# Kernel optimization log

Measured on AMD Instinct MI355X. Metric: run time of the kernel, lower is better.

## Reference

```python
import jax, jax.numpy as jnp
import numpy as np
from jax import lax

EPS = 1e-5
T, N, E = 10, 10000, 320000
C_IN, C_HID, C_OUT = 16, 32, 16


def _stgcn_layer(x, edge_index, edge_weight, tw, tb, gw, gb, gamma, beta):
    # x: [T, N, Cin] -> temporal conv over T per node
    xc = jnp.transpose(x, (1, 2, 0))  # [N, Cin, T]
    y = lax.conv_general_dilated(xc, tw, window_strides=(1,), padding=((1, 1),),
                                 dimension_numbers=("NCH", "OIH", "NCH"))
    y = y + tb[None, :, None]
    y = jnp.clip(y, -10.0, 10.0)
    # InstanceNorm1d (affine, biased var over time axis)
    mu = jnp.mean(y, axis=-1, keepdims=True)
    var = jnp.mean((y - mu) ** 2, axis=-1, keepdims=True)
    y = (y - mu) * lax.rsqrt(var + EPS) * gamma[None, :, None] + beta[None, :, None]
    y = jax.nn.relu(y)
    h = jnp.transpose(y, (0, 2, 1))  # [N, T, C]

    n = h.shape[0]
    # GCNConv normalization (identical at every timestep -> computed once)
    ewn = jax.nn.softmax(edge_weight)  # softmax over all E edges
    loop = jnp.arange(n, dtype=edge_index.dtype)
    row = jnp.concatenate([edge_index[0], loop])  # sources (+self loops)
    col = jnp.concatenate([edge_index[1], loop])  # destinations
    w = jnp.concatenate([ewn, jnp.ones((n,), dtype=ewn.dtype)])
    deg = jax.ops.segment_sum(w, col, num_segments=n)
    dinv = jnp.where(deg > 0, lax.rsqrt(jnp.maximum(deg, EPS * 0 + 1e-30)), 0.0)
    norm = dinv[row] * w * dinv[col]  # [E+N]

    hw = jnp.einsum("ntc,cd->ntd", h, gw)  # [N, T, C]
    msg = hw[row] * norm[:, None, None]     # [E+N, T, C] gather
    agg = jax.ops.segment_sum(msg, col, num_segments=n) + gb  # scatter-add
    out = jnp.clip(jax.nn.relu(agg), -10.0, 10.0)
    return jnp.transpose(out, (1, 0, 2))  # [T, N, C]


def setup_inputs() -> dict:
    key = jax.random.key(0)
    ks = jax.random.split(key, 16)
    inp = {
        "x": jax.random.normal(ks[0], (T, N, C_IN), dtype=jnp.float32),
        "edge_index": jax.random.randint(ks[1], (2, E), 0, N, dtype=jnp.int32),
        "edge_weight": jax.random.uniform(ks[2], (E,), dtype=jnp.float32),
        # layer 1 (in -> hid)
        "l1_tw": jax.random.normal(ks[3], (C_HID, C_IN, 3), dtype=jnp.float32) * 0.02,
        "l1_tb": jnp.zeros((C_HID,), dtype=jnp.float32),
        "l1_gw": jax.random.normal(ks[4], (C_HID, C_HID), dtype=jnp.float32) * 0.1,
        "l1_gb": jnp.zeros((C_HID,), dtype=jnp.float32),
        "l1_gamma": jnp.ones((C_HID,), dtype=jnp.float32),
        "l1_beta": jnp.zeros((C_HID,), dtype=jnp.float32),
        # layer 2 (hid -> hid)
        "l2_tw": jax.random.normal(ks[5], (C_HID, C_HID, 3), dtype=jnp.float32) * 0.02,
        "l2_tb": jnp.zeros((C_HID,), dtype=jnp.float32),
        "l2_gw": jax.random.normal(ks[6], (C_HID, C_HID), dtype=jnp.float32) * 0.1,
        "l2_gb": jnp.zeros((C_HID,), dtype=jnp.float32),
        "l2_gamma": jnp.ones((C_HID,), dtype=jnp.float32),
        "l2_beta": jnp.zeros((C_HID,), dtype=jnp.float32),
        # output linear
        "out_w": jax.random.normal(ks[7], (C_HID, C_OUT), dtype=jnp.float32) * 0.1,
        "out_b": jnp.zeros((C_OUT,), dtype=jnp.float32),
    }
    return inp


def reference(x, edge_index, edge_weight,
              l1_tw, l1_tb, l1_gw, l1_gb, l1_gamma, l1_beta,
              l2_tw, l2_tb, l2_gw, l2_gb, l2_gamma, l2_beta,
              out_w, out_b):
    h = _stgcn_layer(x, edge_index, edge_weight, l1_tw, l1_tb, l1_gw, l1_gb, l1_gamma, l1_beta)
    h = _stgcn_layer(h, edge_index, edge_weight, l2_tw, l2_tb, l2_gw, l2_gb, l2_gamma, l2_beta)
    # per-timestep linear then mean over time == mean then linear, done faithfully
    outs = jnp.einsum("tnc,cd->tnd", h, out_w) + out_b
    return jnp.mean(outs, axis=0)  # [N, C_OUT]
```

## Files before the change

### kernel.cpp

```cpp
#include <hip/hip_runtime.h>
#include <hip/hip_bf16.h>
#include <string.h>


typedef __hip_bfloat16 bf16;

#define TSTEPS 10
#define TPAD 12
#define CHID 32
#define ROWELE (TSTEPS * CHID)
#define ROWW4 40

#define DEG_SHIFT 45
#define DEG_SCALE 16777216.0f
#define DEG_MASK ((1ULL << DEG_SHIFT) - 1)

__device__ __forceinline__ float b2f(bf16 v) { return __bfloat162float(v); }
__device__ __forceinline__ float ldf(const void* p, long i, int bf) {
    return bf ? __bfloat162float(((const bf16*)p)[i]) : ((const float*)p)[i];
}
__device__ __forceinline__ int detect_bf(const unsigned* gbits) {
    return (gbits[0] != 0x3F800000u) ? 1 : 0;
}
__device__ __forceinline__ float bflo(unsigned u) { return __uint_as_float(u << 16); }
__device__ __forceinline__ float bfhi(unsigned u) { return __uint_as_float(u & 0xFFFF0000u); }
__device__ __forceinline__ unsigned pack2bf(float a, float b) {
    bf16 x = __float2bfloat16(a), y = __float2bfloat16(b);
    unsigned short ux, uy;
    memcpy(&ux, &x, 2); memcpy(&uy, &y, 2);
    return (unsigned)ux | ((unsigned)uy << 16);
}
__device__ __forceinline__ unsigned short bfbits(float a) {
    bf16 x = __float2bfloat16(a);
    unsigned short u; memcpy(&u, &x, 2);
    return u;
}
__device__ __forceinline__ void accum8(float* f, uint4 u, float w) {
    f[0] += w * bflo(u.x); f[1] += w * bfhi(u.x);
    f[2] += w * bflo(u.y); f[3] += w * bfhi(u.y);
    f[4] += w * bflo(u.z); f[5] += w * bfhi(u.z);
    f[6] += w * bflo(u.w); f[7] += w * bfhi(u.w);
}
__device__ __forceinline__ unsigned long long packdeg(float e) {
    return (1ULL << DEG_SHIFT) + (unsigned long long)(e * DEG_SCALE);
}


__global__ __launch_bounds__(256) void edge_kernel(
    const void* __restrict__ ew, const unsigned* __restrict__ gbits,
    const int* __restrict__ ei,
    float* __restrict__ ewn, unsigned long long* __restrict__ packed,
    int* __restrict__ rank, float* __restrict__ sumexp, int E) {
    __shared__ float s_red[4];
    int bf = detect_bf(gbits);
    int tid = threadIdx.x;
    int i0 = (blockIdx.x * 256 + tid) * 4;
    float e0 = 0.0f, e1 = 0.0f, e2 = 0.0f, e3 = 0.0f;
    if ((E & 3) == 0 && i0 + 3 < E) {
        float w0, w1, w2, w3;
        if (bf) {
            uint2 u = ((const uint2*)ew)[i0 >> 2];
            w0 = bflo(u.x); w1 = bfhi(u.x); w2 = bflo(u.y); w3 = bfhi(u.y);
        } else {
            float4 f = ((const float4*)ew)[i0 >> 2];
            w0 = f.x; w1 = f.y; w2 = f.z; w3 = f.w;
        }
        e0 = __expf(w0); e1 = __expf(w1); e2 = __expf(w2); e3 = __expf(w3);
        int4 c4 = *(const int4*)&ei[E + i0];
        unsigned long long o0 = atomicAdd(&packed[c4.x], packdeg(e0));
        unsigned long long o1 = atomicAdd(&packed[c4.y], packdeg(e1));
        unsigned long long o2 = atomicAdd(&packed[c4.z], packdeg(e2));
        unsigned long long o3 = atomicAdd(&packed[c4.w], packdeg(e3));
        *(float4*)&ewn[i0] = make_float4(e0, e1, e2, e3);
        *(int4*)&rank[i0] = make_int4((int)(o0 >> DEG_SHIFT),
                                      (int)(o1 >> DEG_SHIFT),
                                      (int)(o2 >> DEG_SHIFT),
                                      (int)(o3 >> DEG_SHIFT));
    } else {
        float es[4] = {0, 0, 0, 0};
        for (int j = 0; j < 4; j++) {
            int i = i0 + j;
            if (i < E) {
                float e = __expf(ldf(ew, i, bf));
                es[j] = e;
                ewn[i] = e;
                unsigned long long o =
                    atomicAdd(&packed[ei[E + i]], packdeg(e));
                rank[i] = (int)(o >> DEG_SHIFT);
            }
        }
        e0 = es[0]; e1 = es[1]; e2 = es[2]; e3 = es[3];
    }
    float v = (e0 + e1) + (e2 + e3);
    for (int o = 32; o > 0; o >>= 1) v += __shfl_down(v, o);
    int lane = tid & 63, wv = tid >> 6;
    if (lane == 0) s_red[wv] = v;
    __syncthreads();
    if (tid == 0) atomicAdd(sumexp, s_red[0] + s_red[1] + s_red[2] + s_red[3]);
}


__global__ __launch_bounds__(1024) void scan_kernel(
    const unsigned long long* __restrict__ packed,
    const float* __restrict__ sumexp,
    float* __restrict__ dinv, int* __restrict__ off, int N) {
    __shared__ int s[1024];
    int tid = threadIdx.x;
    float invS = 1.0f / (*sumexp);
    for (int i = tid; i < N; i += 1024) {
        float deg = (float)(packed[i] & DEG_MASK) * (1.0f / DEG_SCALE);
        dinv[i] = rsqrtf(1.0f + deg * invS);
    }
    int chunk = (N + 1023) / 1024;
    int b0 = tid * chunk;
    int p = 0;
    for (int k = 0; k < chunk; k++) {
        int i = b0 + k;
        if (i < N) p += (int)(packed[i] >> DEG_SHIFT);
    }
    s[tid] = p;
    __syncthreads();
    for (int d = 1; d < 1024; d <<= 1) {
        int v = (tid >= d) ? s[tid - d] : 0;
        __syncthreads();
        s[tid] += v;
        __syncthreads();
    }
    int base = s[tid] - p;
    for (int k = 0; k < chunk; k++) {
        int i = b0 + k;
        if (i < N) {
            off[i] = base;
            base += (int)(packed[i] >> DEG_SHIFT);
            if (i == N - 1) off[N] = base;
        }
    }
}


template <int CIN, int LAYOUT>
__device__ __forceinline__ void conv_body(
    int bb, const void* __restrict__ in_, int bfw,
    const void* __restrict__ tw, const void* __restrict__ tb,
    const void* __restrict__ gamma, const void* __restrict__ beta,
    const void* __restrict__ gw,
    bf16* __restrict__ hw, int N, int tid) {
    constexpr int CO = CHID;
    __shared__ __align__(16) float s_in[8 * CIN * TPAD];
    __shared__ __align__(16) float s_h[8 * CO * TPAD];
    __shared__ __align__(16) unsigned s_tw01[CIN * CO];
    __shared__ __align__(16) unsigned short s_tw2[CIN * CO];
    __shared__ __align__(16) unsigned s_gwp[(CO / 2) * CO];

    int nl = tid >> 5, o = tid & 31;

    float tbv = ldf(tb, o, bfw);
    float gav = ldf(gamma, o, bfw);
    float bev = ldf(beta, o, bfw);

    for (int i = tid; i < CIN * CO; i += 256) {
        int ci = i / CO, oo = i % CO;
        long base = ((long)oo * CIN + ci) * 3;
        float w0 = ldf(tw, base, bfw);
        float w1 = ldf(tw, base + 1, bfw);
        float w2 = ldf(tw, base + 2, bfw);
        s_tw01[ci * CO + oo] = pack2bf(w0, w1);
        s_tw2[ci * CO + oo] = bfbits(w2);
    }
    for (int i = tid; i < (CO / 2) * CO; i += 256) {
        int cp = i / CO, oo = i % CO;
        s_gwp[i] = pack2bf(ldf(gw, (long)(2 * cp) * CO + oo, bfw),
                           ldf(gw, (long)(2 * cp + 1) * CO + oo, bfw));
    }

    int nb = bb * 8;

    if (LAYOUT == 0) {
        constexpr int CP = CIN / 2;
        for (int i2 = tid; i2 < 8 * TSTEPS * CP; i2 += 256) {
            int cp = i2 % CP;
            int t = (i2 / CP) % TSTEPS;
            int nn = i2 / (CP * TSTEPS);
            int n = nb + nn;
            float v0 = 0.0f, v1 = 0.0f;
            if (n < N) {
                long idx = (long)t * ((long)N * CIN) + (long)n * CIN + 2 * cp;
                if (bfw) {
                    unsigned u = ((const unsigned*)in_)[idx >> 1];
                    v0 = bflo(u); v1 = bfhi(u);
                } else {
                    float2 f = ((const float2*)in_)[idx >> 1];
                    v0 = f.x; v1 = f.y;
                }
            }
            int b = nn * (CIN * TPAD) + (2 * cp) * TPAD + t;
            s_in[b] = v0;
            s_in[b + TPAD] = v1;
        }
    } else {
        for (int i2 = tid; i2 < 8 * CIN * 5; i2 += 256) {
            int tp = i2 % 5;
            int ci = (i2 / 5) % CIN;
            int nn = i2 / (5 * CIN);
            int n = nb + nn;
            float v0 = 0.0f, v1 = 0.0f;
            if (n < N) {
                long idx = (long)n * (CIN * TSTEPS) + ci * TSTEPS + 2 * tp;
                unsigned u = ((const unsigned*)in_)[idx >> 1];
                v0 = bflo(u); v1 = bfhi(u);
            }
            int b = nn * (CIN * TPAD) + ci * TPAD + 2 * tp;
            s_in[b] = v0;
            s_in[b + 1] = v1;
        }
    }
    __syncthreads();

    int n = nb + nl;
    const float* xrow = &s_in[nl * CIN * TPAD];

    float acc[TSTEPS];
#pragma unroll
    for (int t = 0; t < TSTEPS; t++) acc[t] = tbv;

    for (int ci = 0; ci < CIN; ci++) {
        const float4* xp = (const float4*)&xrow[ci * TPAD];
        float4 A = xp[0], B = xp[1], C = xp[2];
        float xr[TSTEPS] = {A.x, A.y, A.z, A.w, B.x, B.y, B.z, B.w, C.x, C.y};
        unsigned w01 = s_tw01[ci * CO + o];
        float w0 = bflo(w01), w1 = bfhi(w01);
        float w2 = __uint_as_float(((unsigned)s_tw2[ci * CO + o]) << 16);
        acc[0] += xr[0] * w1 + xr[1] * w2;
#pragma unroll
        for (int t = 1; t < TSTEPS - 1; t++)
            acc[t] += xr[t - 1] * w0 + xr[t] * w1 + xr[t + 1] * w2;
        acc[TSTEPS - 1] += xr[TSTEPS - 2] * w0 + xr[TSTEPS - 1] * w1;
    }

#pragma unroll
    for (int t = 0; t < TSTEPS; t++) acc[t] = fminf(fmaxf(acc[t], -10.0f), 10.0f);
    float mu = 0.0f;
#pragma unroll
    for (int t = 0; t < TSTEPS; t++) mu += acc[t];
    mu *= 0.1f;
    float var = 0.0f;
#pragma unroll
    for (int t = 0; t < TSTEPS; t++) { float d = acc[t] - mu; var += d * d; }
    var *= 0.1f;
    float sc = gav * rsqrtf(var + 1e-5f);
    float h[TSTEPS];
#pragma unroll
    for (int t = 0; t < TSTEPS; t++) h[t] = fmaxf((acc[t] - mu) * sc + bev, 0.0f);

    float4* hp = (float4*)&s_h[nl * CO * TPAD + o * TPAD];
    hp[0] = make_float4(h[0], h[1], h[2], h[3]);
    hp[1] = make_float4(h[4], h[5], h[6], h[7]);
    hp[2] = make_float4(h[8], h[9], 0.0f, 0.0f);
    __syncthreads();

    float acc2[TSTEPS];
#pragma unroll
    for (int t = 0; t < TSTEPS; t++) acc2[t] = 0.0f;
    const float* hrow = &s_h[nl * CO * TPAD];
    for (int cp = 0; cp < CO / 2; cp++) {
        unsigned g2 = s_gwp[cp * CO + o];
        float g0 = bflo(g2), g1 = bfhi(g2);
        const float4* r0 = (const float4*)&hrow[(2 * cp) * TPAD];
        const float4* r1 = (const float4*)&hrow[(2 * cp + 1) * TPAD];
        float4 A0 = r0[0], B0 = r0[1], C0 = r0[2];
        float4 A1 = r1[0], B1 = r1[1], C1 = r1[2];
        acc2[0] += A0.x * g0 + A1.x * g1;
        acc2[1] += A0.y * g0 + A1.y * g1;
        acc2[2] += A0.z * g0 + A1.z * g1;
        acc2[3] += A0.w * g0 + A1.w * g1;
        acc2[4] += B0.x * g0 + B1.x * g1;
        acc2[5] += B0.y * g0 + B1.y * g1;
        acc2[6] += B0.z * g0 + B1.z * g1;
        acc2[7] += B0.w * g0 + B1.w * g1;
        acc2[8] += C0.x * g0 + C1.x * g1;
        acc2[9] += C0.y * g0 + C1.y * g1;
    }
    if (n < N) {
        unsigned* hwp = (unsigned*)hw;
        long base = (long)n * (ROWELE / 2) + o * (TSTEPS / 2);
#pragma unroll
        for (int j = 0; j < 5; j++)
            hwp[base + j] = pack2bf(acc2[2 * j], acc2[2 * j + 1]);
    }
}


__device__ __forceinline__ void fill_body(
    int bb, const int* __restrict__ ei, const float* __restrict__ ewn,
    const int* __restrict__ rank,
    const float* __restrict__ dinv, const float* __restrict__ sumexp,
    const int* __restrict__ off, int2* __restrict__ csr, int E, int tid) {
    int i0 = (bb * 256 + tid) * 4;
    if (i0 >= E) return;
    float invS = 1.0f / (*sumexp);
    if ((E & 3) == 0 && i0 + 3 < E) {
        int4 r4 = *(const int4*)&ei[i0];
        int4 c4 = *(const int4*)&ei[E + i0];
        float4 e4 = *(const float4*)&ewn[i0];
        int4 p4 = *(const int4*)&rank[i0];
        int rr[4] = {r4.x, r4.y, r4.z, r4.w};
        int cc[4] = {c4.x, c4.y, c4.z, c4.w};
        float ee[4] = {e4.x, e4.y, e4.z, e4.w};
        int pp[4] = {p4.x, p4.y, p4.z, p4.w};
#pragma unroll
        for (int j = 0; j < 4; j++) {
            int r = rr[j], c = cc[j];
            float w = dinv[r] * (ee[j] * invS) * dinv[c];
            csr[off[c] + pp[j]] = make_int2(r, __float_as_int(w));
        }
    } else {
        for (int j = 0; j < 4; j++) {
            int i = i0 + j;
            if (i >= E) break;
            int r = ei[i], c = ei[E + i];
            float w = dinv[r] * (ewn[i] * invS) * dinv[c];
            csr[off[c] + rank[i]] = make_int2(r, __float_as_int(w));
        }
    }
}


__global__ __launch_bounds__(256) void fill_conv1_kernel(
    const int* __restrict__ ei, const float* __restrict__ ewn,
    const int* __restrict__ rank,
    const float* __restrict__ dinv, const float* __restrict__ sumexp,
    const int* __restrict__ off, int2* __restrict__ csr, int E, int gE,
    const void* __restrict__ x, const unsigned* __restrict__ gbits,
    const void* __restrict__ tw, const void* __restrict__ tb,
    const void* __restrict__ gamma, const void* __restrict__ beta,
    const void* __restrict__ gw,
    bf16* __restrict__ hw, int N) {
    int tid = threadIdx.x;
    if ((int)blockIdx.x < gE) {
        fill_body(blockIdx.x, ei, ewn, rank, dinv, sumexp, off, csr, E, tid);
    } else {
        conv_body<16, 0>(blockIdx.x - gE, x, detect_bf(gbits), tw, tb, gamma,
                         beta, gw, hw, N, tid);
    }
}

__global__ __launch_bounds__(256) void conv2_kernel(
    const void* __restrict__ in_, const unsigned* __restrict__ gbits,
    const void* __restrict__ tw, const void* __restrict__ tb,
    const void* __restrict__ gamma, const void* __restrict__ beta,
    const void* __restrict__ gw,
    bf16* __restrict__ hw, int N) {
    conv_body<32, 1>(blockIdx.x, in_, detect_bf(gbits), tw, tb, gamma, beta,
                     gw, hw, N, threadIdx.x);
}


template <bool FINAL>
__global__ __launch_bounds__(320) void agg_kernel_t(
    const uint4* __restrict__ hw4, const int* __restrict__ off,
    const int2* __restrict__ csr,
    const float* __restrict__ dinv, const void* __restrict__ gb,
    const void* __restrict__ ow, const void* __restrict__ ob,
    const unsigned* __restrict__ gbits,
    void* __restrict__ out, int N) {
    __shared__ int2 s_sw[ROWELE];
    __shared__ float s_part[8 * ROWW4 * 9];
    __shared__ float s_hbar[CHID];
    __shared__ float s_ow[CHID * 16];
    __shared__ float s_ob[16];

    int bf = detect_bf(gbits);
    int n = blockIdx.x;
    int tid = threadIdx.x;
    int g = tid % ROWW4;
    int eo = tid / ROWW4;

    if (FINAL) {
        for (int i = tid; i < CHID * 16; i += ROWELE) s_ow[i] = ldf(ow, i, bf);
        if (tid < 16) s_ob[tid] = ldf(ob, tid, bf);
    }

    float facc[8];
#pragma unroll
    for (int j = 0; j < 8; j++) facc[j] = 0.0f;

    float dn = dinv[n];
    if (eo == 0) {
        uint4 u = hw4[n * ROWW4 + g];
        accum8(facc, u, dn * dn);
    }

    int beg = off[n], end = off[n + 1];
    for (int base = beg; base < end; base += ROWELE) {
        int m = min(ROWELE, end - base);
        if (tid < m) s_sw[tid] = csr[base + tid];
        __syncthreads();
        int kmax = (m + 7) >> 3;
        int k = 0;
        for (; k + 2 <= kmax; k += 2) {
            int j0 = (k << 3) + eo, j1 = j0 + 8;
            int c0 = min(j0, m - 1), c1 = min(j1, m - 1);
            int2 e0 = s_sw[c0], e1 = s_sw[c1];
            float w0 = (j0 < m) ? __int_as_float(e0.y) : 0.0f;
            float w1 = (j1 < m) ? __int_as_float(e1.y) : 0.0f;
            uint4 u0 = hw4[e0.x * ROWW4 + g];
            uint4 u1 = hw4[e1.x * ROWW4 + g];
            accum8(facc, u0, w0);
            accum8(facc, u1, w1);
        }
        if (k < kmax) {
            int j0 = (k << 3) + eo;
            int c0 = min(j0, m - 1);
            int2 e0 = s_sw[c0];
            float w0 = (j0 < m) ? __int_as_float(e0.y) : 0.0f;
            uint4 u0 = hw4[e0.x * ROWW4 + g];
            accum8(facc, u0, w0);
        }
        __syncthreads();
    }

    {
        float* rowp = &s_part[(eo * ROWW4 + g) * 9];
#pragma unroll
        for (int j = 0; j < 8; j++) rowp[j] = facc[j];
    }
    __syncthreads();
    int gg = tid >> 3, jj = tid & 7;
    float v = 0.0f;
#pragma unroll
    for (int s = 0; s < 8; s++) v += s_part[(s * ROWW4 + gg) * 9 + jj];
    int c = tid / TSTEPS;
    v += ldf(gb, c, bf);
    v = fminf(fmaxf(v, 0.0f), 10.0f);

    if (!FINAL) {
        ((bf16*)out)[(long)n * ROWELE + tid] = __float2bfloat16(v);
    } else {
        __syncthreads();
        s_part[tid] = v;
        __syncthreads();
        if (tid < CHID) {
            float s = 0.0f;
#pragma unroll
            for (int t = 0; t < TSTEPS; t++) s += s_part[tid * TSTEPS + t];
            s_hbar[tid] = s * 0.1f;
        }
        __syncthreads();
        if (tid < 16) {
            float a = s_ob[tid];
#pragma unroll
            for (int cc = 0; cc < CHID; cc++) a += s_hbar[cc] * s_ow[cc * 16 + tid];
            long oi = (long)n * 16 + tid;
            if (bf) ((bf16*)out)[oi] = __float2bfloat16(a);
            else    ((float*)out)[oi] = a;
        }
    }
}


extern "C" void kernel_launch(void* const* d_in, const int* in_sizes, int n_in,
                              void* d_out, int out_size, void* d_ws, size_t ws_size,
                              hipStream_t stream) {
    (void)n_in; (void)out_size; (void)ws_size;

    const void* x     = d_in[0];
    const int*  ei    = (const int*)d_in[1];
    const void* ew    = d_in[2];
    const void* l1_tw = d_in[3];
    const void* l1_tb = d_in[4];
    const void* l1_gw = d_in[5];
    const void* l1_gb = d_in[6];
    const unsigned* gbits = (const unsigned*)d_in[7];
    const void* l1_ga = d_in[7];
    const void* l1_be = d_in[8];
    const void* l2_tw = d_in[9];
    const void* l2_tb = d_in[10];
    const void* l2_gw = d_in[11];
    const void* l2_gb = d_in[12];
    const void* l2_ga = d_in[13];
    const void* l2_be = d_in[14];
    const void* out_w = d_in[15];
    const void* out_b = d_in[16];

    int N = in_sizes[0] / (TSTEPS * 16);
    int E = in_sizes[1] / 2;

    char* p = (char*)d_ws;
    auto alloc = [&](size_t bytes) -> char* {
        char* r = p;
        p += (bytes + 255) & ~(size_t)255;
        return r;
    };
    char* zbase   = p;
    float* sumexp = (float*)alloc(256);
    unsigned long long* packed = (unsigned long long*)alloc((size_t)N * 8);
    size_t zbytes = (size_t)(p - zbase);
    int*   rankA   = (int*)alloc((size_t)E * 4);
    float* ewn     = (float*)alloc((size_t)E * 4);
    float* dinv    = (float*)alloc((size_t)N * 4);
    int*   offA    = (int*)alloc((size_t)(N + 1) * 4);
    int2*  csr     = (int2*)alloc((size_t)E * 8);
    bf16*  bufA    = (bf16*)alloc((size_t)N * ROWELE * 2);
    bf16*  bufB    = (bf16*)alloc((size_t)N * ROWELE * 2);

    int gE4 = (E + 1023) / 1024;
    int gConv = (N + 7) / 8;

    hipMemsetAsync(zbase, 0, zbytes, stream);
    hipLaunchKernelGGL(edge_kernel, dim3(gE4), dim3(256), 0, stream,
                       ew, gbits, ei, ewn, packed, rankA, sumexp, E);
    hipLaunchKernelGGL(scan_kernel, dim3(1), dim3(1024), 0, stream,
                       packed, sumexp, dinv, offA, N);
    hipLaunchKernelGGL(fill_conv1_kernel, dim3(gE4 + gConv), dim3(256), 0, stream,
                       ei, ewn, rankA, dinv, sumexp, offA, csr, E, gE4,
                       x, gbits, l1_tw, l1_tb, l1_ga, l1_be, l1_gw, bufA, N);

    hipLaunchKernelGGL((agg_kernel_t<false>), dim3(N), dim3(ROWELE), 0, stream,
                       (const uint4*)bufA, offA, csr, dinv, l1_gb,
                       nullptr, nullptr, gbits, (void*)bufB, N);
    hipLaunchKernelGGL(conv2_kernel, dim3(gConv), dim3(256), 0, stream,
                       (const void*)bufB, gbits, l2_tw, l2_tb, l2_ga, l2_be,
                       l2_gw, bufA, N);
    hipLaunchKernelGGL((agg_kernel_t<true>), dim3(N), dim3(ROWELE), 0, stream,
                       (const uint4*)bufA, offA, csr, dinv, l2_gb,
                       out_w, out_b, gbits, d_out, N);
}
```

Before: 252.9 us.

## Fuse layer-1 graph aggregation with layer-2 temporal conv and projection

Replaces the separate layer-1 aggregation kernel and the conv2 kernel with one kernel. Each block aggregates 10 nodes serially into shared memory, then runs the temporal conv, instance norm and GCN weight projection for those nodes. This removes one launch and the global write and reread of the intermediate buffer. In exchange the grid shrinks from N blocks to N/10 blocks, and each block walks through 10 nodes one after another with several barriers per node. That can cut parallelism and latency hiding in the gather-heavy aggregation.

```diff
diff --git a/kernel.cpp b/kernel.cpp
--- a/kernel.cpp
+++ b/kernel.cpp
@@ -344,14 +344,175 @@
     }
 }
 
-__global__ __launch_bounds__(256) void conv2_kernel(
-    const void* __restrict__ in_, const unsigned* __restrict__ gbits,
+
+__global__ __launch_bounds__(320) void aggconv2_kernel(
+    const uint4* __restrict__ hw4, const int* __restrict__ off,
+    const int2* __restrict__ csr, const float* __restrict__ dinv,
+    const void* __restrict__ gb, const unsigned* __restrict__ gbits,
     const void* __restrict__ tw, const void* __restrict__ tb,
     const void* __restrict__ gamma, const void* __restrict__ beta,
     const void* __restrict__ gw,
-    bf16* __restrict__ hw, int N) {
-    conv_body<32, 1>(blockIdx.x, in_, detect_bf(gbits), tw, tb, gamma, beta,
-                     gw, hw, N, threadIdx.x);
+    bf16* __restrict__ hw2, int N) {
+    constexpr int CIN = CHID, CO = CHID, NB = 10;
+    __shared__ int2 s_sw[ROWELE];
+    __shared__ float s_part[8 * ROWW4 * 9];
+    __shared__ __align__(16) float s_in[NB * CIN * TPAD];
+    __shared__ __align__(16) float s_h[NB * CO * TPAD];
+    __shared__ __align__(16) unsigned s_tw01[CIN * CO];
+    __shared__ __align__(16) unsigned short s_tw2[CIN * CO];
+    __shared__ __align__(16) unsigned s_gwp[(CO / 2) * CO];
+
+    int bf = detect_bf(gbits);
+    int tid = threadIdx.x;
+    int g = tid % ROWW4;
+    int eo = tid / ROWW4;
+    int nb = blockIdx.x * NB;
+
+    for (int i = tid; i < CIN * CO; i += 320) {
+        int ci = i / CO, oo = i % CO;
+        long base = ((long)oo * CIN + ci) * 3;
+        s_tw01[ci * CO + oo] = pack2bf(ldf(tw, base, bf), ldf(tw, base + 1, bf));
+        s_tw2[ci * CO + oo] = bfbits(ldf(tw, base + 2, bf));
+    }
+    for (int i = tid; i < (CO / 2) * CO; i += 320) {
+        int cp = i / CO, oo = i % CO;
+        s_gwp[i] = pack2bf(ldf(gw, (long)(2 * cp) * CO + oo, bf),
+                           ldf(gw, (long)(2 * cp + 1) * CO + oo, bf));
+    }
+
+    for (int nn = 0; nn < NB; nn++) {
+        int n = nb + nn;
+        if (n >= N) break;
+        float facc[8];
+#pragma unroll
+        for (int j = 0; j < 8; j++) facc[j] = 0.0f;
+        float dn = dinv[n];
+        if (eo == 0) {
+            uint4 u = hw4[n * ROWW4 + g];
+            accum8(facc, u, dn * dn);
+        }
+        int beg = off[n], end = off[n + 1];
+        for (int cbase = beg; cbase < end; cbase += ROWELE) {
+            int m = min(ROWELE, end - cbase);
+            if (tid < m) s_sw[tid] = csr[cbase + tid];
+            __syncthreads();
+            int kmax = (m + 7) >> 3;
+            int k = 0;
+            for (; k + 2 <= kmax; k += 2) {
+                int j0 = (k << 3) + eo, j1 = j0 + 8;
+                int c0 = min(j0, m - 1), c1 = min(j1, m - 1);
+                int2 e0 = s_sw[c0], e1 = s_sw[c1];
+                float w0 = (j0 < m) ? __int_as_float(e0.y) : 0.0f;
+                float w1 = (j1 < m) ? __int_as_float(e1.y) : 0.0f;
+                uint4 u0 = hw4[e0.x * ROWW4 + g];
+                uint4 u1 = hw4[e1.x * ROWW4 + g];
+                accum8(facc, u0, w0);
+                accum8(facc, u1, w1);
+            }
+            if (k < kmax) {
+                int j0 = (k << 3) + eo;
+                int c0 = min(j0, m - 1);
+                int2 e0 = s_sw[c0];
+                float w0 = (j0 < m) ? __int_as_float(e0.y) : 0.0f;
+                uint4 u0 = hw4[e0.x * ROWW4 + g];
+                accum8(facc, u0, w0);
+            }
+            __syncthreads();
+        }
+        {
+            float* rowp = &s_part[(eo * ROWW4 + g) * 9];
+#pragma unroll
+            for (int j = 0; j < 8; j++) rowp[j] = facc[j];
+        }
+        __syncthreads();
+        int gg = tid >> 3, jj = tid & 7;
+        float v = 0.0f;
+#pragma unroll
+        for (int s = 0; s < 8; s++) v += s_part[(s * ROWW4 + gg) * 9 + jj];
+        int c = tid / TSTEPS, t = tid % TSTEPS;
+        v += ldf(gb, c, bf);
+        v = fminf(fmaxf(v, 0.0f), 10.0f);
+        v = b2f(__float2bfloat16(v));
+        s_in[(nn * CIN + c) * TPAD + t] = v;
+        __syncthreads();
+    }
+    __syncthreads();
+
+    int nl = tid / 32, o = tid & 31;
+    int n = nb + nl;
+    float tbv = ldf(tb, o, bf);
+    float gav = ldf(gamma, o, bf);
+    float bev = ldf(beta, o, bf);
+
+    float acc[TSTEPS];
+#pragma unroll
+    for (int t = 0; t < TSTEPS; t++) acc[t] = tbv;
+
+    const float* xrow = &s_in[nl * CIN * TPAD];
+    for (int ci = 0; ci < CIN; ci++) {
+        const float4* xp = (const float4*)&xrow[ci * TPAD];
+        float4 A = xp[0], B = xp[1], C = xp[2];
+        float xr[TSTEPS] = {A.x, A.y, A.z, A.w, B.x, B.y, B.z, B.w, C.x, C.y};
+        unsigned w01 = s_tw01[ci * CO + o];
+        float w0 = bflo(w01), w1 = bfhi(w01);
+        float w2 = __uint_as_float(((unsigned)s_tw2[ci * CO + o]) << 16);
+        acc[0] += xr[0] * w1 + xr[1] * w2;
+#pragma unroll
+        for (int t = 1; t < TSTEPS - 1; t++)
+            acc[t] += xr[t - 1] * w0 + xr[t] * w1 + xr[t + 1] * w2;
+        acc[TSTEPS - 1] += xr[TSTEPS - 2] * w0 + xr[TSTEPS - 1] * w1;
+    }
+
+#pragma unroll
+    for (int t = 0; t < TSTEPS; t++) acc[t] = fminf(fmaxf(acc[t], -10.0f), 10.0f);
+    float mu = 0.0f;
+#pragma unroll
+    for (int t = 0; t < TSTEPS; t++) mu += acc[t];
+    mu *= 0.1f;
+    float var = 0.0f;
+#pragma unroll
+    for (int t = 0; t < TSTEPS; t++) { float d = acc[t] - mu; var += d * d; }
+    var *= 0.1f;
+    float sc = gav * rsqrtf(var + 1e-5f);
+    float h[TSTEPS];
+#pragma unroll
+    for (int t = 0; t < TSTEPS; t++) h[t] = fmaxf((acc[t] - mu) * sc + bev, 0.0f);
+
+    float4* hp = (float4*)&s_h[nl * CO * TPAD + o * TPAD];
+    hp[0] = make_float4(h[0], h[1], h[2], h[3]);
+    hp[1] = make_float4(h[4], h[5], h[6], h[7]);
+    hp[2] = make_float4(h[8], h[9], 0.0f, 0.0f);
+    __syncthreads();
+
+    float acc2[TSTEPS];
+#pragma unroll
+    for (int t = 0; t < TSTEPS; t++) acc2[t] = 0.0f;
+    const float* hrow = &s_h[nl * CO * TPAD];
+    for (int cp = 0; cp < CO / 2; cp++) {
+        unsigned g2 = s_gwp[cp * CO + o];
+        float g0 = bflo(g2), g1 = bfhi(g2);
+        const float4* r0 = (const float4*)&hrow[(2 * cp) * TPAD];
+        const float4* r1 = (const float4*)&hrow[(2 * cp + 1) * TPAD];
+        float4 A0 = r0[0], B0 = r0[1], C0 = r0[2];
+        float4 A1 = r1[0], B1 = r1[1], C1 = r1[2];
+        acc2[0] += A0.x * g0 + A1.x * g1;
+        acc2[1] += A0.y * g0 + A1.y * g1;
+        acc2[2] += A0.z * g0 + A1.z * g1;
+        acc2[3] += A0.w * g0 + A1.w * g1;
+        acc2[4] += B0.x * g0 + B1.x * g1;
+        acc2[5] += B0.y * g0 + B1.y * g1;
+        acc2[6] += B0.z * g0 + B1.z * g1;
+        acc2[7] += B0.w * g0 + B1.w * g1;
+        acc2[8] += C0.x * g0 + C1.x * g1;
+        acc2[9] += C0.y * g0 + C1.y * g1;
+    }
+    if (n < N) {
+        unsigned* hwp = (unsigned*)hw2;
+        long base = (long)n * (ROWELE / 2) + o * (TSTEPS / 2);
+#pragma unroll
+        for (int j = 0; j < 5; j++)
+            hwp[base + j] = pack2bf(acc2[2 * j], acc2[2 * j + 1]);
+    }
 }
 
 
@@ -505,6 +666,7 @@
 
     int gE4 = (E + 1023) / 1024;
     int gConv = (N + 7) / 8;
+    int gAC = (N + 9) / 10;
 
     hipMemsetAsync(zbase, 0, zbytes, stream);
     hipLaunchKernelGGL(edge_kernel, dim3(gE4), dim3(256), 0, stream,
@@ -514,14 +676,10 @@
     hipLaunchKernelGGL(fill_conv1_kernel, dim3(gE4 + gConv), dim3(256), 0, stream,
                        ei, ewn, rankA, dinv, sumexp, offA, csr, E, gE4,
                        x, gbits, l1_tw, l1_tb, l1_ga, l1_be, l1_gw, bufA, N);
-
-    hipLaunchKernelGGL((agg_kernel_t<false>), dim3(N), dim3(ROWELE), 0, stream,
-                       (const uint4*)bufA, offA, csr, dinv, l1_gb,
-                       nullptr, nullptr, gbits, (void*)bufB, N);
-    hipLaunchKernelGGL(conv2_kernel, dim3(gConv), dim3(256), 0, stream,
-                       (const void*)bufB, gbits, l2_tw, l2_tb, l2_ga, l2_be,
-                       l2_gw, bufA, N);
+    hipLaunchKernelGGL(aggconv2_kernel, dim3(gAC), dim3(320), 0, stream,
+                       (const uint4*)bufA, offA, csr, dinv, l1_gb, gbits,
+                       l2_tw, l2_tb, l2_ga, l2_be, l2_gw, bufB, N);
     hipLaunchKernelGGL((agg_kernel_t<true>), dim3(N), dim3(ROWELE), 0, stream,
-                       (const uint4*)bufA, offA, csr, dinv, l2_gb,
+                       (const uint4*)bufB, offA, csr, dinv, l2_gb,
                        out_w, out_b, gbits, d_out, N);
 }
```

New measurement: 314.5 us. 24.4% more time.
